# Kernel optimization log

Hardware: AMD Instinct MI355X
Metric: run time of the kernel (lower is better)

## Reference

```python
import jax, jax.numpy as jnp
import numpy as np
from jax.ops import segment_sum, segment_max

N, D, B = 1536, 32, 8            # nodes, candidate out-degree per node, sequential batch steps
OBS, HID, HEADS, C = 33, 64, 4, 8  # obs_dim, GRU hidden, attn heads, out_dim//heads
E = N * D


def setup_inputs() -> dict:
    key = jax.random.key(0)
    ks = jax.random.split(key, 16)
    g = lambda i, shape, s=0.1: jax.random.normal(ks[i], shape, jnp.float32) * s
    src = jnp.repeat(jnp.arange(N), D)                    # uniform degree -> scatter_topk = row top-k
    dst = jax.random.randint(ks[0], (E,), 0, N)
    return dict(
        H_t=jax.random.normal(ks[1], (B, N, OBS), jnp.float32),
        src=src, dst=dst, k=4,
        W_e1=g(2, (OBS, 32)), b_e1=jnp.zeros(32), W_e2=g(3, (32, 32)), b_e2=jnp.zeros(32),
        ln_g=jnp.ones(32), ln_b=jnp.zeros(32),
        W_ih=g(4, (3 * HID, 32)), W_hh=g(5, (3 * HID, HID)),
        b_ih=jnp.zeros(3 * HID), b_hh=jnp.zeros(3 * HID),
        W_s1=g(6, (2 * HID, 64)), b_s1=jnp.zeros(64), W_s2=g(7, (64, 1)), b_s2=jnp.zeros(1),
        W_gat=g(8, (HID, HEADS * C)), att_src=g(9, (HEADS, C)), att_dst=g(10, (HEADS, C)),
        b_gat=jnp.zeros(HEADS * C),
    )


def _layernorm(x, g, b, eps=1e-5):
    mu = x.mean(-1, keepdims=True)
    var = ((x - mu) ** 2).mean(-1, keepdims=True)
    return (x - mu) * jax.lax.rsqrt(var + eps) * g + b


def _forward(H_t, src, dst, k, W_e1, b_e1, W_e2, b_e2, ln_g, ln_b,
             W_ih, W_hh, b_ih, b_hh, W_s1, b_s1, W_s2, b_s2,
             W_gat, att_src, att_dst, b_gat):
    # ObsEmbedding: Linear-ReLU-Linear-ReLU-LayerNorm, applied to all (B,N) at once
    x = jax.nn.relu(H_t @ W_e1 + b_e1)
    x = jax.nn.relu(x @ W_e2 + b_e2)
    H_emb = _layernorm(x, ln_g, ln_b)              # (B,N,32)

    def step(h, e_t):
        # --- NodeMemory: shared GRUCell, h carried across batch steps ---
        gi = e_t @ W_ih.T + b_ih                   # (N,3H)
        gh = h @ W_hh.T + b_hh
        i_r, i_z, i_n = jnp.split(gi, 3, -1)
        h_r, h_z, h_n = jnp.split(gh, 3, -1)
        r = jax.nn.sigmoid(i_r + h_r)
        z = jax.nn.sigmoid(i_z + h_z)
        n = jnp.tanh(i_n + r * h_n)
        h_new = (1.0 - z) * n + z * h              # (N,HID)

        # --- EdgeScorer: sigmoid MLP score per candidate edge, keep top-k per source ---
        feat = jnp.concatenate([h_new[src], h_new[dst]], -1)        # (E,2*HID)
        score = jax.nn.sigmoid(
            (jax.nn.relu(feat @ W_s1 + b_s1) @ W_s2 + b_s2)[:, 0])  # (E,)
        s2 = score.reshape(N, D)
        top_idx = jax.lax.top_k(s2, k)[1]                           # (N,k)
        keep = (jnp.zeros((N, D), bool)
                .at[jnp.arange(N)[:, None], top_idx].set(True)).reshape(-1)  # (E,)
        w = jnp.where(keep, score, 0.0)                             # soft edge weights

        # --- GATConv (add_self_loops=False), pruned edges masked out of the softmax ---
        xh = (h_new @ W_gat).reshape(N, HEADS, C)
        a_s = (xh * att_src).sum(-1)               # (N,HEADS)
        a_d = (xh * att_dst).sum(-1)
        logit = jax.nn.leaky_relu(a_s[src] + a_d[dst], 0.2)         # (E,HEADS)
        logit = jnp.where(keep[:, None], logit, -1e30)
        m = segment_max(logit, dst, num_segments=N)                 # softmax grouped by target
        ex = jnp.where(keep[:, None], jnp.exp(logit - m[dst]), 0.0)
        ssum = segment_sum(ex, dst, num_segments=N)
        alpha = ex / jnp.clip(ssum[dst], 1e-16)                     # (E,HEADS)

        msg = alpha[:, :, None] * xh[src] * w[:, None, None]        # edge_weight scales messages
        out = segment_sum(msg, dst, num_segments=N).reshape(N, HEADS * C) + b_gat

        # --- densify attention: scatter-accumulate then row-normalize ---
        A = jnp.zeros((HEADS, N, N), alpha.dtype).at[:, src, dst].add(alpha.T)
        A = A / jnp.clip(A.sum(-1, keepdims=True), 1e-9)
        return h_new, (out, A)

    h0 = jnp.zeros((N, HID), H_t.dtype)
    _, (outs, attns) = jax.lax.scan(step, h0, H_emb)
    return outs, attns                              # (B,N,32), (B,HEADS,N,N)


def reference(H_t, src, dst, k, W_e1, b_e1, W_e2, b_e2, ln_g, ln_b,
              W_ih, W_hh, b_ih, b_hh, W_s1, b_s1, W_s2, b_s2,
              W_gat, att_src, att_dst, b_gat):
    return _forward(H_t, src, dst, k, W_e1, b_e1, W_e2, b_e2, ln_g, ln_b,
                    W_ih, W_hh, b_ih, b_hh, W_s1, b_s1, W_s2, b_s2,
                    W_gat, att_src, att_dst, b_gat)
```

## Files before the change

kernel.cpp:

```cpp
#include <hip/hip_runtime.h>
#include <math.h>

#define NN   1536
#define DG   32
#define BB   8
#define OBSD 33
#define HID  64
#define NHEAD 4
#define EE   (NN*DG)

__device__ __forceinline__ float sigm(float x){ return 1.0f/(1.0f+expf(-x)); }
__device__ __forceinline__ float rl(float v, int l){
    return __int_as_float(__builtin_amdgcn_readlane(__float_as_int(v), l));
}

__global__ void __launch_bounds__(256) k_embgi(
                      const float* __restrict__ Ht,
                      const float* __restrict__ We1, const float* __restrict__ be1,
                      const float* __restrict__ We2, const float* __restrict__ be2,
                      const float* __restrict__ lng, const float* __restrict__ lnb,
                      const float* __restrict__ Wih, const float* __restrict__ bih,
                      float* __restrict__ GI){
    __shared__ float lwih[192*33];
    int tid = threadIdx.x;
    for(int i=tid;i<192*32;i+=256){ int r=i>>5, c=i&31; lwih[r*33+c]=Wih[i]; }
    __syncthreads();
    int lane = tid & 63;
    int j32 = lane & 31;
    int bn = blockIdx.x*4 + (tid>>6);
    const float* hrow = Ht + (size_t)bn*OBSD;
    float x1 = be1[j32];
    for(int o=0;o<OBSD;o++) x1 += hrow[o]*We1[o*32+j32];
    x1 = fmaxf(x1,0.f);
    float x2 = be2[j32];
    for(int i=0;i<32;i++){
        float xi = rl(x1, i);
        x2 += xi * We2[i*32+j32];
    }
    x2 = fmaxf(x2,0.f);
    float mu = x2;
    for(int m=16;m>=1;m>>=1) mu += __shfl_xor(mu, m, 32);
    mu *= (1.0f/32.0f);
    float d = x2-mu; float var = d*d;
    for(int m=16;m>=1;m>>=1) var += __shfl_xor(var, m, 32);
    var *= (1.0f/32.0f);
    float xln = d*rsqrtf(var+1e-5f)*lng[j32]+lnb[j32];
    int j = lane;
    float gr=bih[j], gz=bih[64+j], gn=bih[128+j];
    for(int kk=0;kk<32;kk++){
        float ek = rl(xln, kk);
        gr += ek*lwih[j*33+kk];
        gz += ek*lwih[(64+j)*33+kk];
        gn += ek*lwih[(128+j)*33+kk];
    }
    float* g = GI + (size_t)bn*192;
    g[j]=gr; g[64+j]=gz; g[128+j]=gn;
}

__global__ void k_count(const int* __restrict__ dst, int* __restrict__ cursor){
    int e = blockIdx.x*256+threadIdx.x;
    if(e<EE) atomicAdd(&cursor[dst[e]],1);
}
__global__ void k_scan(int* __restrict__ cnt, int* __restrict__ indptr){
    __shared__ int part[256];
    int t = threadIdx.x;
    int local[6]; int s=0;
    for(int i=0;i<6;i++){ local[i]=cnt[t*6+i]; s+=local[i]; }
    part[t]=s; __syncthreads();
    if(t==0){ int acc=0; for(int i=0;i<256;i++){ int v=part[i]; part[i]=acc; acc+=v; } }
    __syncthreads();
    int pre = part[t];
    for(int i=0;i<6;i++){ int idx=t*6+i; indptr[idx]=pre; cnt[idx]=pre; pre+=local[i]; }
    if(t==255) indptr[NN]=EE;
}
__global__ void k_fill(const int* __restrict__ dst, int* __restrict__ cursor, int* __restrict__ eids){
    int e = blockIdx.x*256+threadIdx.x;
    if(e<EE){ int p = atomicAdd(&cursor[dst[e]],1); eids[p]=e; }
}

__global__ void __launch_bounds__(384) k_gru_all(const float* __restrict__ GI,
                       const float* __restrict__ Whh, const float* __restrict__ bhh,
                       float* __restrict__ Hall){
    __shared__ float lw[192*65];
    int tid = threadIdx.x;
    for(int i=tid;i<192*64;i+=384){ int r=i>>6, c=i&63; lw[r*65+c]=Whh[i]; }
    __syncthreads();
    int node = blockIdx.x*6 + (tid>>6);
    int j = tid&63;
    float b_r=bhh[j], b_z=bhh[64+j], b_n=bhh[128+j];
    const float* lwr = lw + j*65;
    const float* lwz = lw + (64+j)*65;
    const float* lwn = lw + (128+j)*65;
    float hold = 0.f;
    for(int t=0;t<BB;t++){
        float hr=b_r, hz=b_z, hn=b_n;
        for(int kk=0;kk<64;kk++){
            float hk = rl(hold,kk);
            hr += hk*lwr[kk];
            hz += hk*lwz[kk];
            hn += hk*lwn[kk];
        }
        const float* g = GI + ((size_t)t*NN+node)*192;
        float r  = sigm(g[j]     + hr);
        float z  = sigm(g[64+j]  + hz);
        float nn_= tanhf(g[128+j] + r*hn);
        hold = (1.f-z)*nn_ + z*hold;
        Hall[((size_t)t*NN+node)*64 + j] = hold;
    }
}

__global__ void __launch_bounds__(256) k_post(const float* __restrict__ Hall,
                       const float* __restrict__ Ws1, const float* __restrict__ Wgat,
                       const float* __restrict__ atts, const float* __restrict__ attd,
                       float* __restrict__ P, float* __restrict__ Q,
                       float* __restrict__ xh, float* __restrict__ as_, float* __restrict__ ad_){
    __shared__ float ws1l[128*64];
    __shared__ float wgl[64*32];
    int tid = threadIdx.x;
    for(int i=tid;i<128*64;i+=256) ws1l[i]=Ws1[i];
    for(int i=tid;i<64*32;i+=256)  wgl[i]=Wgat[i];
    __syncthreads();
    int bn = blockIdx.x*4 + (tid>>6);
    int j = tid&63;
    float hv = Hall[(size_t)bn*64+j];
    float p=0.f,q=0.f,xv=0.f;
    for(int kk=0;kk<64;kk++){
        float hk=rl(hv,kk);
        p += hk*ws1l[kk*64+j];
        q += hk*ws1l[(64+kk)*64+j];
        if(j<32) xv += hk*wgl[kk*32+j];
    }
    P[(size_t)bn*64+j]=p; Q[(size_t)bn*64+j]=q;
    if(j<32){
        xh[(size_t)bn*32+j]=xv;
        float asv = xv*atts[j];
        float adv = xv*attd[j];
        for(int m=1;m<8;m<<=1){ asv += __shfl_xor(asv,m); adv += __shfl_xor(adv,m); }
        if((j&7)==0){ as_[(size_t)bn*4+(j>>3)]=asv; ad_[(size_t)bn*4+(j>>3)]=adv; }
    }
}

__global__ void k_edge(const float* __restrict__ P, const float* __restrict__ Q,
                       const float* __restrict__ bs1, const float* __restrict__ Ws2,
                       const float* __restrict__ bs2, const int* __restrict__ dst,
                       const int* __restrict__ kptr, float* __restrict__ wbuf){
    int lane = threadIdx.x;
    int t = blockIdx.y;
    int row = blockIdx.x*2 + (lane>>5);
    int d = lane & 31;
    int e = row*DG + d;
    int de = dst[e];
    const float4* Pr = (const float4*)(P + ((size_t)t*NN+row)*64);
    const float4* Qr = (const float4*)(Q + ((size_t)t*NN+de)*64);
    const float4* B1 = (const float4*)bs1;
    const float4* W2 = (const float4*)Ws2;
    float acc = 0.f;
    #pragma unroll
    for(int jj=0;jj<16;jj++){
        float4 pv=Pr[jj], qv=Qr[jj], bv=B1[jj], wv=W2[jj];
        acc += fmaxf(pv.x+qv.x+bv.x,0.f)*wv.x;
        acc += fmaxf(pv.y+qv.y+bv.y,0.f)*wv.y;
        acc += fmaxf(pv.z+qv.z+bv.z,0.f)*wv.z;
        acc += fmaxf(pv.w+qv.w+bv.w,0.f)*wv.w;
    }
    float score = sigm(acc + bs2[0]);
    int kk = kptr[0]; if(kk>32) kk=32; if(kk<0) kk=0;
    bool sel=false;
    for(int it=0; it<kk; it++){
        float v = sel ? -INFINITY : score;
        int idx = d;
        for(int m=16;m>=1;m>>=1){
            float ov = __shfl_xor(v,m,32);
            int   oi = __shfl_xor(idx,m,32);
            if(ov>v || (ov==v && oi<idx)){ v=ov; idx=oi; }
        }
        if(idx==d) sel=true;
    }
    wbuf[(size_t)t*EE + e] = sel ? score : 0.f;
}

__global__ void __launch_bounds__(256) k_soft(const int* __restrict__ indptr, const int* __restrict__ eids,
                       const int* __restrict__ src,
                       const float* __restrict__ as_, const float* __restrict__ ad_,
                       const float* __restrict__ wbuf, const float* __restrict__ xhb,
                       const float* __restrict__ bgat,
                       float* __restrict__ alphab, float* __restrict__ outp){
    int t = blockIdx.y;
    int n = blockIdx.x*4 + (threadIdx.x>>6);
    int lane = threadIdx.x & 63;
    const float*  w    = wbuf + (size_t)t*EE;
    const float4* as4  = (const float4*)(as_ + (size_t)t*NN*4);
    const float4* ad4v = (const float4*)(ad_ + (size_t)t*NN*4);
    const float*  xhbt = xhb + (size_t)t*NN*32;
    float4* alpha      = (float4*)(alphab + (size_t)t*EE*4);
    int beg = indptr[n], end = indptr[n+1];
    float4 adq = ad4v[n];
    float adv[4] = {adq.x, adq.y, adq.z, adq.w};

    int   i0 = beg + lane, i1 = beg + 64 + lane;
    int   e0 = 0, e1 = 0, s0 = 0, s1 = 0;
    float w0 = 0.f, w1 = 0.f;
    float av0[4]={0.f,0.f,0.f,0.f}, av1[4]={0.f,0.f,0.f,0.f};
    if(i0 < end){
        e0 = eids[i0]; w0 = w[e0];
        if(w0>0.f){ s0 = src[e0]; float4 qv = as4[s0]; av0[0]=qv.x;av0[1]=qv.y;av0[2]=qv.z;av0[3]=qv.w; }
    }
    if(i1 < end){
        e1 = eids[i1]; w1 = w[e1];
        if(w1>0.f){ s1 = src[e1]; float4 qv = as4[s1]; av1[0]=qv.x;av1[1]=qv.y;av1[2]=qv.z;av1[3]=qv.w; }
    }
    float lg0[4], lg1[4], m[4];
    #pragma unroll
    for(int h=0;h<4;h++){
        float l0 = av0[h]+adv[h]; l0 = l0>0.f ? l0 : 0.2f*l0;
        float l1 = av1[h]+adv[h]; l1 = l1>0.f ? l1 : 0.2f*l1;
        lg0[h] = (w0>0.f) ? l0 : -INFINITY;
        lg1[h] = (w1>0.f) ? l1 : -INFINITY;
        m[h] = fmaxf(lg0[h], lg1[h]);
    }
    bool tail = (end - beg) > 128;
    if(tail){
        for(int i=beg+128+lane; i<end; i+=64){
            int e=eids[i]; float wv=w[e];
            if(wv>0.f){
                float4 qv = as4[src[e]];
                float qa[4]={qv.x,qv.y,qv.z,qv.w};
                #pragma unroll
                for(int h=0;h<4;h++){ float l=qa[h]+adv[h]; l=l>0.f?l:0.2f*l; m[h]=fmaxf(m[h],l); }
            }
        }
    }
    #pragma unroll
    for(int mm=32;mm>=1;mm>>=1){
        #pragma unroll
        for(int h=0;h<4;h++) m[h] = fmaxf(m[h], __shfl_xor(m[h], mm));
    }
    float ex0[4], ex1[4], ss[4];
    #pragma unroll
    for(int h=0;h<4;h++){
        ex0[h] = (w0>0.f) ? expf(lg0[h]-m[h]) : 0.f;
        ex1[h] = (w1>0.f) ? expf(lg1[h]-m[h]) : 0.f;
        ss[h]  = ex0[h]+ex1[h];
    }
    if(tail){
        for(int i=beg+128+lane; i<end; i+=64){
            int e=eids[i]; float wv=w[e];
            float exq[4]={0.f,0.f,0.f,0.f};
            if(wv>0.f){
                float4 qv = as4[src[e]];
                float qa[4]={qv.x,qv.y,qv.z,qv.w};
                #pragma unroll
                for(int h=0;h<4;h++){ float l=qa[h]+adv[h]; l=l>0.f?l:0.2f*l; exq[h]=expf(l-m[h]); ss[h]+=exq[h]; }
            }
            alpha[e] = make_float4(exq[0],exq[1],exq[2],exq[3]);
        }
    }
    #pragma unroll
    for(int mm=32;mm>=1;mm>>=1){
        #pragma unroll
        for(int h=0;h<4;h++) ss[h] += __shfl_xor(ss[h], mm);
    }
    float inv[4];
    #pragma unroll
    for(int h=0;h<4;h++) inv[h] = 1.0f/fmaxf(ss[h],1e-16f);

    float acc[32];
    #pragma unroll
    for(int c=0;c<32;c++) acc[c]=0.f;

    if(i0 < end){
        float a0[4];
        #pragma unroll
        for(int h=0;h<4;h++) a0[h]=ex0[h]*inv[h];
        alpha[e0] = make_float4(a0[0],a0[1],a0[2],a0[3]);
        if(w0>0.f){
            const float4* xr4 = (const float4*)(xhbt + (size_t)s0*32);
            #pragma unroll
            for(int h=0;h<4;h++){
                float aw = a0[h]*w0;
                float4 xa = xr4[h*2], xb = xr4[h*2+1];
                acc[h*8+0]+=aw*xa.x; acc[h*8+1]+=aw*xa.y; acc[h*8+2]+=aw*xa.z; acc[h*8+3]+=aw*xa.w;
                acc[h*8+4]+=aw*xb.x; acc[h*8+5]+=aw*xb.y; acc[h*8+6]+=aw*xb.z; acc[h*8+7]+=aw*xb.w;
            }
        }
    }
    if(i1 < end){
        float a1[4];
        #pragma unroll
        for(int h=0;h<4;h++) a1[h]=ex1[h]*inv[h];
        alpha[e1] = make_float4(a1[0],a1[1],a1[2],a1[3]);
        if(w1>0.f){
            const float4* xr4 = (const float4*)(xhbt + (size_t)s1*32);
            #pragma unroll
            for(int h=0;h<4;h++){
                float aw = a1[h]*w1;
                float4 xa = xr4[h*2], xb = xr4[h*2+1];
                acc[h*8+0]+=aw*xa.x; acc[h*8+1]+=aw*xa.y; acc[h*8+2]+=aw*xa.z; acc[h*8+3]+=aw*xa.w;
                acc[h*8+4]+=aw*xb.x; acc[h*8+5]+=aw*xb.y; acc[h*8+6]+=aw*xb.z; acc[h*8+7]+=aw*xb.w;
            }
        }
    }
    if(tail){
        for(int i=beg+128+lane; i<end; i+=64){
            int e=eids[i]; float wv=w[e];
            float4 qv = alpha[e];
            float a[4]={qv.x*inv[0], qv.y*inv[1], qv.z*inv[2], qv.w*inv[3]};
            alpha[e] = make_float4(a[0],a[1],a[2],a[3]);
            if(wv>0.f){
                const float4* xr4 = (const float4*)(xhbt + (size_t)src[e]*32);
                #pragma unroll
                for(int h=0;h<4;h++){
                    float aw = a[h]*wv;
                    float4 xa = xr4[h*2], xb = xr4[h*2+1];
                    acc[h*8+0]+=aw*xa.x; acc[h*8+1]+=aw*xa.y; acc[h*8+2]+=aw*xa.z; acc[h*8+3]+=aw*xa.w;
                    acc[h*8+4]+=aw*xb.x; acc[h*8+5]+=aw*xb.y; acc[h*8+6]+=aw*xb.z; acc[h*8+7]+=aw*xb.w;
                }
            }
        }
    }
    #pragma unroll
    for(int mm=32;mm>=1;mm>>=1){
        #pragma unroll
        for(int c=0;c<32;c++) acc[c] += __shfl_xor(acc[c], mm);
    }
    if(lane==0){
        float4* o = (float4*)(outp + ((size_t)t*NN+n)*32);
        const float4* bg4 = (const float4*)bgat;
        #pragma unroll
        for(int q8=0;q8<8;q8++){
            float4 b = bg4[q8];
            o[q8] = make_float4(acc[q8*4]+b.x, acc[q8*4+1]+b.y, acc[q8*4+2]+b.z, acc[q8*4+3]+b.w);
        }
    }
}

__global__ void __launch_bounds__(256) k_scatter(const float* __restrict__ alphab,
                       const int* __restrict__ dst, float* __restrict__ attn){
    __shared__ float rowbuf[NHEAD][NN];
    __shared__ float rs[NHEAD];
    __shared__ float rsf[NHEAD];
    int n = blockIdx.x;
    int t = blockIdx.y;
    const float* alpha = alphab + (size_t)t*EE*4;
    int tid = threadIdx.x;
    for(int i=tid;i<NHEAD*(NN/4);i+=256) ((float4*)rowbuf)[i]=make_float4(0.f,0.f,0.f,0.f);
    if(tid<NHEAD) rs[tid]=0.f;
    __syncthreads();
    float a=0.f; int de=0; int h=0;
    if(tid<128){
        int d = tid>>2; h = tid&3;
        int e = n*DG+d;
        a = alpha[e*4+h];
        de = dst[e];
        if(a>0.f) atomicAdd(&rs[h], a);
    }
    __syncthreads();
    if(tid<NHEAD) rsf[tid] = 1.0f/fmaxf(rs[tid],1e-9f);
    __syncthreads();
    if(tid<128 && a>0.f) atomicAdd(&rowbuf[h][de], a*rsf[h]);
    __syncthreads();
    size_t tb = (size_t)t*NHEAD*NN*NN;
    for(int i=tid;i<NHEAD*(NN/4);i+=256){
        int hh = i/(NN/4); int c4 = i%(NN/4);
        float4 v = ((const float4*)rowbuf[hh])[c4];
        ((float4*)(attn + tb + (size_t)hh*NN*NN + (size_t)n*NN))[c4] = v;
    }
}

extern "C" void kernel_launch(void* const* d_in, const int* in_sizes, int n_in,
                              void* d_out, int out_size, void* d_ws, size_t ws_size,
                              hipStream_t stream) {
    const float* Ht   = (const float*)d_in[0];
    const int*   src  = (const int*)  d_in[1];
    const int*   dst  = (const int*)  d_in[2];
    const int*   kptr = (const int*)  d_in[3];
    const float* We1  = (const float*)d_in[4];
    const float* be1  = (const float*)d_in[5];
    const float* We2  = (const float*)d_in[6];
    const float* be2  = (const float*)d_in[7];
    const float* lng  = (const float*)d_in[8];
    const float* lnb  = (const float*)d_in[9];
    const float* Wih  = (const float*)d_in[10];
    const float* Whh  = (const float*)d_in[11];
    const float* bih  = (const float*)d_in[12];
    const float* bhh  = (const float*)d_in[13];
    const float* Ws1  = (const float*)d_in[14];
    const float* bs1  = (const float*)d_in[15];
    const float* Ws2  = (const float*)d_in[16];
    const float* bs2  = (const float*)d_in[17];
    const float* Wgat = (const float*)d_in[18];
    const float* atts = (const float*)d_in[19];
    const float* attd = (const float*)d_in[20];
    const float* bgat = (const float*)d_in[21];

    float* outp = (float*)d_out;
    float* attn = outp + (size_t)BB*NN*32;

    float* ws    = (float*)d_ws;
    float* GI    = ws;
    float* Hall  = ws + 2359296;
    float* P     = ws + 3145728;
    float* Q     = ws + 3932160;
    float* xh    = ws + 4718592;
    float* as_   = ws + 5111808;
    float* ad_   = ws + 5160960;
    float* wbuf  = ws + 5210112;
    float* alpha = ws + 5603328;
    int*   ibase = (int*)(ws + 7176192);
    int*   cursor= ibase;
    int*   indptr= ibase + 2048;
    int*   eids  = ibase + 4096;

    hipMemsetAsync(cursor, 0, (size_t)NN*sizeof(int), stream);

    k_embgi<<<BB*NN/4, 256, 0, stream>>>(Ht, We1, be1, We2, be2, lng, lnb, Wih, bih, GI);
    k_count<<<EE/256, 256, 0, stream>>>(dst, cursor);
    k_scan<<<1, 256, 0, stream>>>(cursor, indptr);
    k_fill<<<EE/256, 256, 0, stream>>>(dst, cursor, eids);
    k_gru_all<<<NN/6, 384, 0, stream>>>(GI, Whh, bhh, Hall);
    k_post<<<BB*NN/4, 256, 0, stream>>>(Hall, Ws1, Wgat, atts, attd, P, Q, xh, as_, ad_);
    {
        dim3 g(NN/2, BB);
        k_edge<<<g, 64, 0, stream>>>(P, Q, bs1, Ws2, bs2, dst, kptr, wbuf);
    }
    {
        dim3 gs(NN/4, BB);
        k_soft<<<gs, 256, 0, stream>>>(indptr, eids, src, as_, ad_, wbuf, xh, bgat, alpha, outp);
        dim3 g(NN, BB);
        k_scatter<<<g, 256, 0, stream>>>(alpha, dst, attn);
    }
}
```

Before: 490.0 us.

## Fuse embedding, GRU and projections into one kernel; bucket edges by destination

Merges the observation embedding, GRU input projection, recurrent GRU and post-projection (P, Q, xh, attention logits) into a single per-node kernel that loops over time steps, removing the GI and Hall intermediate buffers and several launches. Replaces the count/scan/fill CSR construction with a single atomic bucketing pass into fixed-size per-destination slots, and drops the softmax tail path for degrees above 128. This trades launch overhead and intermediate memory traffic for a serialized, lower-parallelism fused kernel with large shared memory, and assumes in-degree never exceeds 128.

```diff
diff --git a/kernel.cpp b/kernel.cpp
--- a/kernel.cpp
+++ b/kernel.cpp
@@ -8,135 +8,105 @@
 #define HID  64
 #define NHEAD 4
 #define EE   (NN*DG)
+#define MAXDEG 128
 
 __device__ __forceinline__ float sigm(float x){ return 1.0f/(1.0f+expf(-x)); }
 __device__ __forceinline__ float rl(float v, int l){
     return __int_as_float(__builtin_amdgcn_readlane(__float_as_int(v), l));
 }
 
-__global__ void __launch_bounds__(256) k_embgi(
+__global__ void __launch_bounds__(384) k_fused(
                       const float* __restrict__ Ht,
                       const float* __restrict__ We1, const float* __restrict__ be1,
                       const float* __restrict__ We2, const float* __restrict__ be2,
                       const float* __restrict__ lng, const float* __restrict__ lnb,
                       const float* __restrict__ Wih, const float* __restrict__ bih,
-                      float* __restrict__ GI){
+                      const float* __restrict__ Whh, const float* __restrict__ bhh,
+                      const float* __restrict__ Ws1, const float* __restrict__ Wgat,
+                      const float* __restrict__ atts, const float* __restrict__ attd,
+                      float* __restrict__ P, float* __restrict__ Q,
+                      float* __restrict__ xh, float* __restrict__ as_, float* __restrict__ ad_,
+                      int* __restrict__ cursor){
     __shared__ float lwih[192*33];
+    __shared__ float lwhh[192*65];
+    __shared__ float ws1l[128*64];
+    __shared__ float wgl [64*32];
     int tid = threadIdx.x;
-    for(int i=tid;i<192*32;i+=256){ int r=i>>5, c=i&31; lwih[r*33+c]=Wih[i]; }
-    __syncthreads();
-    int lane = tid & 63;
-    int j32 = lane & 31;
-    int bn = blockIdx.x*4 + (tid>>6);
-    const float* hrow = Ht + (size_t)bn*OBSD;
-    float x1 = be1[j32];
-    for(int o=0;o<OBSD;o++) x1 += hrow[o]*We1[o*32+j32];
-    x1 = fmaxf(x1,0.f);
-    float x2 = be2[j32];
-    for(int i=0;i<32;i++){
-        float xi = rl(x1, i);
-        x2 += xi * We2[i*32+j32];
-    }
-    x2 = fmaxf(x2,0.f);
-    float mu = x2;
-    for(int m=16;m>=1;m>>=1) mu += __shfl_xor(mu, m, 32);
-    mu *= (1.0f/32.0f);
-    float d = x2-mu; float var = d*d;
-    for(int m=16;m>=1;m>>=1) var += __shfl_xor(var, m, 32);
-    var *= (1.0f/32.0f);
-    float xln = d*rsqrtf(var+1e-5f)*lng[j32]+lnb[j32];
-    int j = lane;
-    float gr=bih[j], gz=bih[64+j], gn=bih[128+j];
-    for(int kk=0;kk<32;kk++){
-        float ek = rl(xln, kk);
-        gr += ek*lwih[j*33+kk];
-        gz += ek*lwih[(64+j)*33+kk];
-        gn += ek*lwih[(128+j)*33+kk];
-    }
-    float* g = GI + (size_t)bn*192;
-    g[j]=gr; g[64+j]=gz; g[128+j]=gn;
-}
-
-__global__ void k_count(const int* __restrict__ dst, int* __restrict__ cursor){
-    int e = blockIdx.x*256+threadIdx.x;
-    if(e<EE) atomicAdd(&cursor[dst[e]],1);
-}
-__global__ void k_scan(int* __restrict__ cnt, int* __restrict__ indptr){
-    __shared__ int part[256];
-    int t = threadIdx.x;
-    int local[6]; int s=0;
-    for(int i=0;i<6;i++){ local[i]=cnt[t*6+i]; s+=local[i]; }
-    part[t]=s; __syncthreads();
-    if(t==0){ int acc=0; for(int i=0;i<256;i++){ int v=part[i]; part[i]=acc; acc+=v; } }
-    __syncthreads();
-    int pre = part[t];
-    for(int i=0;i<6;i++){ int idx=t*6+i; indptr[idx]=pre; cnt[idx]=pre; pre+=local[i]; }
-    if(t==255) indptr[NN]=EE;
-}
-__global__ void k_fill(const int* __restrict__ dst, int* __restrict__ cursor, int* __restrict__ eids){
-    int e = blockIdx.x*256+threadIdx.x;
-    if(e<EE){ int p = atomicAdd(&cursor[dst[e]],1); eids[p]=e; }
-}
-
-__global__ void __launch_bounds__(384) k_gru_all(const float* __restrict__ GI,
-                       const float* __restrict__ Whh, const float* __restrict__ bhh,
-                       float* __restrict__ Hall){
-    __shared__ float lw[192*65];
-    int tid = threadIdx.x;
-    for(int i=tid;i<192*64;i+=384){ int r=i>>6, c=i&63; lw[r*65+c]=Whh[i]; }
+    if(tid<6) cursor[blockIdx.x*6+tid]=0;
+    for(int i=tid;i<192*32;i+=384){ int r=i>>5, c=i&31; lwih[r*33+c]=Wih[i]; }
+    for(int i=tid;i<192*64;i+=384){ int r=i>>6, c=i&63; lwhh[r*65+c]=Whh[i]; }
+    for(int i=tid;i<128*64;i+=384) ws1l[i]=Ws1[i];
+    for(int i=tid;i<64*32;i+=384)  wgl[i]=Wgat[i];
     __syncthreads();
     int node = blockIdx.x*6 + (tid>>6);
-    int j = tid&63;
-    float b_r=bhh[j], b_z=bhh[64+j], b_n=bhh[128+j];
-    const float* lwr = lw + j*65;
-    const float* lwz = lw + (64+j)*65;
-    const float* lwn = lw + (128+j)*65;
+    int lane = tid&63;
+    int j32  = lane&31;
+    int j    = lane;
+    float bi_r=bih[j], bi_z=bih[64+j], bi_n=bih[128+j];
+    float bh_r=bhh[j], bh_z=bhh[64+j], bh_n=bhh[128+j];
+    const float* lwr = lwhh + j*65;
+    const float* lwz = lwhh + (64+j)*65;
+    const float* lwn = lwhh + (128+j)*65;
     float hold = 0.f;
     for(int t=0;t<BB;t++){
-        float hr=b_r, hz=b_z, hn=b_n;
+        const float* hrow = Ht + ((size_t)t*NN+node)*OBSD;
+        float x1 = be1[j32];
+        for(int o=0;o<OBSD;o++) x1 += hrow[o]*We1[o*32+j32];
+        x1 = fmaxf(x1,0.f);
+        float x2 = be2[j32];
+        for(int i=0;i<32;i++) x2 += rl(x1,i)*We2[i*32+j32];
+        x2 = fmaxf(x2,0.f);
+        float mu = x2;
+        for(int m=16;m>=1;m>>=1) mu += __shfl_xor(mu, m, 32);
+        mu *= (1.0f/32.0f);
+        float d = x2-mu; float var = d*d;
+        for(int m=16;m>=1;m>>=1) var += __shfl_xor(var, m, 32);
+        var *= (1.0f/32.0f);
+        float xln = d*rsqrtf(var+1e-5f)*lng[j32]+lnb[j32];
+        float gr=bi_r, gz=bi_z, gn=bi_n;
+        for(int kk=0;kk<32;kk++){
+            float ek = rl(xln, kk);
+            gr += ek*lwih[j*33+kk];
+            gz += ek*lwih[(64+j)*33+kk];
+            gn += ek*lwih[(128+j)*33+kk];
+        }
+        float hr=bh_r, hz=bh_z, hn=bh_n;
         for(int kk=0;kk<64;kk++){
             float hk = rl(hold,kk);
             hr += hk*lwr[kk];
             hz += hk*lwz[kk];
             hn += hk*lwn[kk];
         }
-        const float* g = GI + ((size_t)t*NN+node)*192;
-        float r  = sigm(g[j]     + hr);
-        float z  = sigm(g[64+j]  + hz);
-        float nn_= tanhf(g[128+j] + r*hn);
+        float r  = sigm(gr + hr);
+        float z  = sigm(gz + hz);
+        float nn_= tanhf(gn + r*hn);
         hold = (1.f-z)*nn_ + z*hold;
-        Hall[((size_t)t*NN+node)*64 + j] = hold;
-    }
-}
-
-__global__ void __launch_bounds__(256) k_post(const float* __restrict__ Hall,
-                       const float* __restrict__ Ws1, const float* __restrict__ Wgat,
-                       const float* __restrict__ atts, const float* __restrict__ attd,
-                       float* __restrict__ P, float* __restrict__ Q,
-                       float* __restrict__ xh, float* __restrict__ as_, float* __restrict__ ad_){
-    __shared__ float ws1l[128*64];
-    __shared__ float wgl[64*32];
-    int tid = threadIdx.x;
-    for(int i=tid;i<128*64;i+=256) ws1l[i]=Ws1[i];
-    for(int i=tid;i<64*32;i+=256)  wgl[i]=Wgat[i];
-    __syncthreads();
-    int bn = blockIdx.x*4 + (tid>>6);
-    int j = tid&63;
-    float hv = Hall[(size_t)bn*64+j];
-    float p=0.f,q=0.f,xv=0.f;
-    for(int kk=0;kk<64;kk++){
-        float hk=rl(hv,kk);
-        p += hk*ws1l[kk*64+j];
-        q += hk*ws1l[(64+kk)*64+j];
-        if(j<32) xv += hk*wgl[kk*32+j];
-    }
-    P[(size_t)bn*64+j]=p; Q[(size_t)bn*64+j]=q;
-    if(j<32){
-        xh[(size_t)bn*32+j]=xv;
-        float asv = xv*atts[j];
-        float adv = xv*attd[j];
-        for(int m=1;m<8;m<<=1){ asv += __shfl_xor(asv,m); adv += __shfl_xor(adv,m); }
-        if((j&7)==0){ as_[(size_t)bn*4+(j>>3)]=asv; ad_[(size_t)bn*4+(j>>3)]=adv; }
+        float p=0.f, q=0.f, xv=0.f;
+        for(int kk=0;kk<64;kk++){
+            float hk = rl(hold,kk);
+            p += hk*ws1l[kk*64+j];
+            q += hk*ws1l[(64+kk)*64+j];
+            if(j<32) xv += hk*wgl[kk*32+j];
+        }
+        size_t bn = (size_t)t*NN+node;
+        P[bn*64+j]=p; Q[bn*64+j]=q;
+        if(j<32){
+            xh[bn*32+j]=xv;
+            float asv = xv*atts[j];
+            float adv = xv*attd[j];
+            for(int m=1;m<8;m<<=1){ asv += __shfl_xor(asv,m); adv += __shfl_xor(adv,m); }
+            if((j&7)==0){ as_[bn*4+(j>>3)]=asv; ad_[bn*4+(j>>3)]=adv; }
+        }
+    }
+}
+
+__global__ void k_group(const int* __restrict__ dst, int* __restrict__ cursor,
+                        int* __restrict__ gedge){
+    int e = blockIdx.x*256+threadIdx.x;
+    if(e<EE){
+        int d = dst[e];
+        int s = atomicAdd(&cursor[d],1);
+        if(s<MAXDEG) gedge[d*MAXDEG+s]=e;
     }
 }
 
@@ -179,7 +149,7 @@
     wbuf[(size_t)t*EE + e] = sel ? score : 0.f;
 }
 
-__global__ void __launch_bounds__(256) k_soft(const int* __restrict__ indptr, const int* __restrict__ eids,
+__global__ void __launch_bounds__(256) k_soft(const int* __restrict__ gcnt, const int* __restrict__ gedge,
                        const int* __restrict__ src,
                        const float* __restrict__ as_, const float* __restrict__ ad_,
                        const float* __restrict__ wbuf, const float* __restrict__ xhb,
@@ -193,20 +163,21 @@
     const float4* ad4v = (const float4*)(ad_ + (size_t)t*NN*4);
     const float*  xhbt = xhb + (size_t)t*NN*32;
     float4* alpha      = (float4*)(alphab + (size_t)t*EE*4);
-    int beg = indptr[n], end = indptr[n+1];
+    int cnt = gcnt[n]; if(cnt>MAXDEG) cnt=MAXDEG;
+    const int* ge = gedge + (size_t)n*MAXDEG;
     float4 adq = ad4v[n];
     float adv[4] = {adq.x, adq.y, adq.z, adq.w};
 
-    int   i0 = beg + lane, i1 = beg + 64 + lane;
     int   e0 = 0, e1 = 0, s0 = 0, s1 = 0;
     float w0 = 0.f, w1 = 0.f;
     float av0[4]={0.f,0.f,0.f,0.f}, av1[4]={0.f,0.f,0.f,0.f};
-    if(i0 < end){
-        e0 = eids[i0]; w0 = w[e0];
+    bool  h0v = lane < cnt, h1v = 64+lane < cnt;
+    if(h0v){
+        e0 = ge[lane]; w0 = w[e0];
         if(w0>0.f){ s0 = src[e0]; float4 qv = as4[s0]; av0[0]=qv.x;av0[1]=qv.y;av0[2]=qv.z;av0[3]=qv.w; }
     }
-    if(i1 < end){
-        e1 = eids[i1]; w1 = w[e1];
+    if(h1v){
+        e1 = ge[64+lane]; w1 = w[e1];
         if(w1>0.f){ s1 = src[e1]; float4 qv = as4[s1]; av1[0]=qv.x;av1[1]=qv.y;av1[2]=qv.z;av1[3]=qv.w; }
     }
     float lg0[4], lg1[4], m[4];
@@ -218,18 +189,6 @@
         lg1[h] = (w1>0.f) ? l1 : -INFINITY;
         m[h] = fmaxf(lg0[h], lg1[h]);
     }
-    bool tail = (end - beg) > 128;
-    if(tail){
-        for(int i=beg+128+lane; i<end; i+=64){
-            int e=eids[i]; float wv=w[e];
-            if(wv>0.f){
-                float4 qv = as4[src[e]];
-                float qa[4]={qv.x,qv.y,qv.z,qv.w};
-                #pragma unroll
-                for(int h=0;h<4;h++){ float l=qa[h]+adv[h]; l=l>0.f?l:0.2f*l; m[h]=fmaxf(m[h],l); }
-            }
-        }
-    }
     #pragma unroll
     for(int mm=32;mm>=1;mm>>=1){
         #pragma unroll
@@ -242,19 +201,6 @@
         ex1[h] = (w1>0.f) ? expf(lg1[h]-m[h]) : 0.f;
         ss[h]  = ex0[h]+ex1[h];
     }
-    if(tail){
-        for(int i=beg+128+lane; i<end; i+=64){
-            int e=eids[i]; float wv=w[e];
-            float exq[4]={0.f,0.f,0.f,0.f};
-            if(wv>0.f){
-                float4 qv = as4[src[e]];
-                float qa[4]={qv.x,qv.y,qv.z,qv.w};
-                #pragma unroll
-                for(int h=0;h<4;h++){ float l=qa[h]+adv[h]; l=l>0.f?l:0.2f*l; exq[h]=expf(l-m[h]); ss[h]+=exq[h]; }
-            }
-            alpha[e] = make_float4(exq[0],exq[1],exq[2],exq[3]);
-        }
-    }
     #pragma unroll
     for(int mm=32;mm>=1;mm>>=1){
         #pragma unroll
@@ -268,7 +214,7 @@
     #pragma unroll
     for(int c=0;c<32;c++) acc[c]=0.f;
 
-    if(i0 < end){
+    if(h0v){
         float a0[4];
         #pragma unroll
         for(int h=0;h<4;h++) a0[h]=ex0[h]*inv[h];
@@ -284,7 +230,7 @@
             }
         }
     }
-    if(i1 < end){
+    if(h1v){
         float a1[4];
         #pragma unroll
         for(int h=0;h<4;h++) a1[h]=ex1[h]*inv[h];
@@ -297,24 +243,6 @@
                 float4 xa = xr4[h*2], xb = xr4[h*2+1];
                 acc[h*8+0]+=aw*xa.x; acc[h*8+1]+=aw*xa.y; acc[h*8+2]+=aw*xa.z; acc[h*8+3]+=aw*xa.w;
                 acc[h*8+4]+=aw*xb.x; acc[h*8+5]+=aw*xb.y; acc[h*8+6]+=aw*xb.z; acc[h*8+7]+=aw*xb.w;
-            }
-        }
-    }
-    if(tail){
-        for(int i=beg+128+lane; i<end; i+=64){
-            int e=eids[i]; float wv=w[e];
-            float4 qv = alpha[e];
-            float a[4]={qv.x*inv[0], qv.y*inv[1], qv.z*inv[2], qv.w*inv[3]};
-            alpha[e] = make_float4(a[0],a[1],a[2],a[3]);
-            if(wv>0.f){
-                const float4* xr4 = (const float4*)(xhbt + (size_t)src[e]*32);
-                #pragma unroll
-                for(int h=0;h<4;h++){
-                    float aw = a[h]*wv;
-                    float4 xa = xr4[h*2], xb = xr4[h*2+1];
-                    acc[h*8+0]+=aw*xa.x; acc[h*8+1]+=aw*xa.y; acc[h*8+2]+=aw*xa.z; acc[h*8+3]+=aw*xa.w;
-                    acc[h*8+4]+=aw*xb.x; acc[h*8+5]+=aw*xb.y; acc[h*8+6]+=aw*xb.z; acc[h*8+7]+=aw*xb.w;
-                }
             }
         }
     }
@@ -397,35 +325,28 @@
     float* attn = outp + (size_t)BB*NN*32;
 
     float* ws    = (float*)d_ws;
-    float* GI    = ws;
-    float* Hall  = ws + 2359296;
-    float* P     = ws + 3145728;
-    float* Q     = ws + 3932160;
-    float* xh    = ws + 4718592;
-    float* as_   = ws + 5111808;
-    float* ad_   = ws + 5160960;
-    float* wbuf  = ws + 5210112;
-    float* alpha = ws + 5603328;
-    int*   ibase = (int*)(ws + 7176192);
+    float* P     = ws;
+    float* Q     = ws +  786432;
+    float* xh    = ws + 1572864;
+    float* as_   = ws + 1966080;
+    float* ad_   = ws + 2015232;
+    float* wbuf  = ws + 2064384;
+    float* alpha = ws + 2457600;
+    int*   ibase = (int*)(ws + 4030464);
     int*   cursor= ibase;
-    int*   indptr= ibase + 2048;
-    int*   eids  = ibase + 4096;
-
-    hipMemsetAsync(cursor, 0, (size_t)NN*sizeof(int), stream);
-
-    k_embgi<<<BB*NN/4, 256, 0, stream>>>(Ht, We1, be1, We2, be2, lng, lnb, Wih, bih, GI);
-    k_count<<<EE/256, 256, 0, stream>>>(dst, cursor);
-    k_scan<<<1, 256, 0, stream>>>(cursor, indptr);
-    k_fill<<<EE/256, 256, 0, stream>>>(dst, cursor, eids);
-    k_gru_all<<<NN/6, 384, 0, stream>>>(GI, Whh, bhh, Hall);
-    k_post<<<BB*NN/4, 256, 0, stream>>>(Hall, Ws1, Wgat, atts, attd, P, Q, xh, as_, ad_);
+    int*   gedge = ibase + 2048;
+
+    k_fused<<<NN/6, 384, 0, stream>>>(Ht, We1, be1, We2, be2, lng, lnb,
+                                      Wih, bih, Whh, bhh, Ws1, Wgat, atts, attd,
+                                      P, Q, xh, as_, ad_, cursor);
+    k_group<<<EE/256, 256, 0, stream>>>(dst, cursor, gedge);
     {
         dim3 g(NN/2, BB);
         k_edge<<<g, 64, 0, stream>>>(P, Q, bs1, Ws2, bs2, dst, kptr, wbuf);
     }
     {
         dim3 gs(NN/4, BB);
-        k_soft<<<gs, 256, 0, stream>>>(indptr, eids, src, as_, ad_, wbuf, xh, bgat, alpha, outp);
+        k_soft<<<gs, 256, 0, stream>>>(cursor, gedge, src, as_, ad_, wbuf, xh, bgat, alpha, outp);
         dim3 g(NN, BB);
         k_scatter<<<g, 256, 0, stream>>>(alpha, dst, attn);
     }
```

Result: slower. 828.2 us (+69.0%).
